# Optimization experiments

Measured on AMD Instinct MI355X. Metric: run time of the kernel, lower is better.

Reference implementation:

```python
import jax, jax.numpy as jnp
import numpy as np

D_IN, N_HEADS, N_KV, HEAD_DIM = 2048, 8, 4, 256
GROUP = N_HEADS // N_KV
SCALING = 256.0 ** -0.5  # query_pre_attn_scalar = 256
EPS = 1e-6


def _rms_norm(x, gamma):
    # Gemma-style RMSNorm with (1 + gamma) scale, over last dim (head_dim)
    var = jnp.mean(x * x, axis=-1, keepdims=True)
    return x * jax.lax.rsqrt(var + EPS) * (1.0 + gamma)


def _apply_rope(x, cos, sin):
    # x: [b, h, s, d]; cos/sin: [s, d] (rotate-half convention)
    d = x.shape[-1]
    x1, x2 = x[..., : d // 2], x[..., d // 2:]
    rotated = jnp.concatenate([-x2, x1], axis=-1)
    return x * cos[None, None] + rotated * sin[None, None]


def setup_inputs() -> dict:
    key = jax.random.key(0)
    ks = jax.random.split(key, 6)
    b, s = 2, 2048
    x = jax.random.normal(ks[0], (b, s, D_IN), dtype=jnp.float32)
    # causal mask: True above diagonal = masked
    mask = jnp.triu(jnp.ones((s, s), dtype=bool), k=1)
    # RoPE tables (base 10000)
    inv_freq = 1.0 / (10000.0 ** (jnp.arange(0, HEAD_DIM, 2, dtype=jnp.float32) / HEAD_DIM))
    angles = jnp.arange(s, dtype=jnp.float32)[:, None] * inv_freq[None, :]  # [s, d/2]
    angles = jnp.concatenate([angles, angles], axis=-1)  # [s, d]
    cos, sin = jnp.cos(angles), jnp.sin(angles)
    std = 0.02
    wq = jax.random.normal(ks[1], (N_HEADS * HEAD_DIM, D_IN), dtype=jnp.float32) * std
    wk = jax.random.normal(ks[2], (N_KV * HEAD_DIM, D_IN), dtype=jnp.float32) * std
    wv = jax.random.normal(ks[3], (N_KV * HEAD_DIM, D_IN), dtype=jnp.float32) * std
    wo = jax.random.normal(ks[4], (D_IN, N_HEADS * HEAD_DIM), dtype=jnp.float32) * std
    q_gamma = jnp.zeros((HEAD_DIM,), dtype=jnp.float32)
    k_gamma = jnp.zeros((HEAD_DIM,), dtype=jnp.float32)
    return {"x": x, "mask": mask, "cos": cos, "sin": sin,
            "wq": wq, "wk": wk, "wv": wv, "wo": wo,
            "q_gamma": q_gamma, "k_gamma": k_gamma}


def reference(x, mask, cos, sin, wq, wk, wv, wo, q_gamma, k_gamma):
    b, s, _ = x.shape
    # projections (torch Linear: y = x @ W.T)
    q = (x @ wq.T).reshape(b, s, N_HEADS, HEAD_DIM).transpose(0, 2, 1, 3)  # [b,H,s,d]
    k = (x @ wk.T).reshape(b, s, N_KV, HEAD_DIM).transpose(0, 2, 1, 3)     # [b,G,s,d]
    v = (x @ wv.T).reshape(b, s, N_KV, HEAD_DIM).transpose(0, 2, 1, 3)     # [b,G,s,d]
    q = _rms_norm(q, q_gamma)
    k = _rms_norm(k, k_gamma)
    q = _apply_rope(q, cos, sin) * SCALING
    k = _apply_rope(k, cos, sin)
    # GQA via broadcast (avoids repeat_interleave): head h = g*GROUP + j (group-major)
    qg = q.reshape(b, N_KV, GROUP, s, HEAD_DIM)
    scores = jnp.einsum('bgjqd,bgkd->bgjqk', qg, k)  # [b,G,group,s,s]
    scores = jnp.where(mask[None, None, None], -jnp.inf, scores)
    weights = jax.nn.softmax(scores, axis=-1)
    ctx = jnp.einsum('bgjqk,bgkd->bgjqd', weights, v)  # [b,G,group,s,d]
    ctx = ctx.reshape(b, N_HEADS, s, HEAD_DIM).transpose(0, 2, 1, 3).reshape(b, s, N_HEADS * HEAD_DIM)
    return ctx @ wo.T
```

## Files before the change

kernel.cpp:

```cpp
#include <hip/hip_runtime.h>
#include <math.h>


typedef __bf16 bf16x8 __attribute__((ext_vector_type(8)));
typedef __bf16 bf16x4 __attribute__((ext_vector_type(4)));
typedef float  f32x4  __attribute__((ext_vector_type(4)));

#define MFMA16(a, b, c) __builtin_amdgcn_mfma_f32_16x16x32_bf16(a, b, c, 0, 0, 0)

__device__ __forceinline__ void async16(const __bf16* g, const __bf16* l) {
  __builtin_amdgcn_global_load_lds(
      (__attribute__((address_space(1))) const void*)g,
      (__attribute__((address_space(3))) void*)l, 16, 0, 0);
}

__global__ __launch_bounds__(256) void cast_f32_bf16(
    const float* __restrict__ src, __bf16* __restrict__ dst) {
  const size_t i = ((size_t)blockIdx.x * 256 + threadIdx.x) * 4;
  f32x4 v = *(const f32x4*)(src + i);
  bf16x4 o;
#pragma unroll
  for (int j = 0; j < 4; j++) o[j] = (__bf16)v[j];
  *(bf16x4*)(dst + i) = o;
}

template <typename OT>
__device__ __forceinline__ void gemm_body(const __bf16* A, const __bf16* B,
                                          OT* C, size_t m0, size_t n0,
                                          size_t ccol0, int ldc) {
  constexpr int K = 2048;
  __shared__ __align__(16) __bf16 As[128 * 32];
  __shared__ __align__(16) __bf16 Bs[128 * 32];
  const int tid = threadIdx.x;
  const int wave = tid >> 6, lane = tid & 63;
  const int lr = lane & 15, lq = lane >> 4;
  const int wm = (wave >> 1) * 64, wn = (wave & 1) * 64;

  f32x4 acc[4][4];
#pragma unroll
  for (int i = 0; i < 4; i++)
#pragma unroll
    for (int j = 0; j < 4; j++)
#pragma unroll
      for (int r = 0; r < 4; r++) acc[i][j][r] = 0.f;

  int srow[2], skof[2];
#pragma unroll
  for (int c = 0; c < 2; c++) {
    const int t = wave * 2 + c;
    const int g = t * 8 + (lane >> 3);
    const int cc = (lane & 7) ^ (g & 7);
    srow[c] = g * 2 + (cc >> 2);
    skof[c] = (cc & 3) * 8;
  }

  for (int k0 = 0; k0 < K; k0 += 32) {
#pragma unroll
    for (int c = 0; c < 2; c++) {
      const int t = wave * 2 + c;
      async16(A + (m0 + srow[c]) * K + k0 + skof[c], As + t * 512);
      async16(B + (n0 + srow[c]) * K + k0 + skof[c], Bs + t * 512);
    }
    __syncthreads();
    bf16x8 af[4], bf[4];
#pragma unroll
    for (int i = 0; i < 4; i++) {
      const int row = wm + i * 16 + lr;
      const int g = row >> 1;
      const int p = ((row & 1) * 4 + lq) ^ (g & 7);
      af[i] = *(const bf16x8*)&As[g * 64 + p * 8];
    }
#pragma unroll
    for (int j = 0; j < 4; j++) {
      const int row = wn + j * 16 + lr;
      const int g = row >> 1;
      const int p = ((row & 1) * 4 + lq) ^ (g & 7);
      bf[j] = *(const bf16x8*)&Bs[g * 64 + p * 8];
    }
#pragma unroll
    for (int i = 0; i < 4; i++)
#pragma unroll
      for (int j = 0; j < 4; j++)
        acc[i][j] = MFMA16(af[i], bf[j], acc[i][j]);
    __syncthreads();
  }

#pragma unroll
  for (int i = 0; i < 4; i++)
#pragma unroll
    for (int j = 0; j < 4; j++)
#pragma unroll
      for (int r = 0; r < 4; r++) {
        const size_t row = m0 + wm + i * 16 + lq * 4 + r;
        const size_t col = ccol0 + wn + j * 16 + lr;
        C[row * (size_t)ldc + col] = (OT)acc[i][j][r];
      }
}

template <typename OT>
__global__ __launch_bounds__(256) void gemm_bt(
    const __bf16* __restrict__ A, const __bf16* __restrict__ B,
    OT* __restrict__ C, const int ldc) {
  gemm_body<OT>(A, B, C, (size_t)blockIdx.y * 128, (size_t)blockIdx.x * 128,
                (size_t)blockIdx.x * 128, ldc);
}

__global__ __launch_bounds__(512, 2) void gemm_qkv8(
    const __bf16* __restrict__ A, const __bf16* __restrict__ Bq,
    const __bf16* __restrict__ Bk, const __bf16* __restrict__ Bv,
    __bf16* __restrict__ C) {
  constexpr int NT = 32;
  __shared__ __align__(16) __bf16 As[2][256 * 64];
  __shared__ __align__(16) __bf16 Bs[2][256 * 64];

  const int bx = blockIdx.x;
  const __bf16* Bg;
  int nl;
  if (bx < 8)       { Bg = Bq; nl = bx; }
  else if (bx < 12) { Bg = Bk; nl = bx - 8; }
  else              { Bg = Bv; nl = bx - 12; }
  const size_t m0 = (size_t)blockIdx.y * 256;
  const size_t n0 = (size_t)nl * 256;
  const size_t ccol0 = (size_t)bx * 256;

  const int tid = threadIdx.x;
  const int wave = tid >> 6, lane = tid & 63;
  const int lr = lane & 15, lq = lane >> 4;
  const int wm = (wave >> 2) * 128, wn = (wave & 3) * 64;

  f32x4 acc[8][4];
#pragma unroll
  for (int i = 0; i < 8; i++)
#pragma unroll
    for (int j = 0; j < 4; j++)
#pragma unroll
      for (int r = 0; r < 4; r++) acc[i][j][r] = 0.f;

  const int srow0 = wave * 8 + (lane >> 3);
  const int sc = ((lane & 7) ^ (srow0 & 7)) * 8;

#define QSTAGE(kt_, nb_)                                                     \
  {                                                                          \
    const int k0_ = (kt_)*64;                                                \
    _Pragma("unroll") for (int s = 0; s < 4; s++) {                          \
      async16(A + (m0 + s * 64 + srow0) * 2048 + k0_ + sc,                   \
              &As[nb_][s * 4096 + wave * 512]);                              \
      async16(Bg + (n0 + s * 64 + srow0) * 2048 + k0_ + sc,                  \
              &Bs[nb_][s * 4096 + wave * 512]);                              \
    }                                                                        \
  }

  QSTAGE(0, 0);
  __syncthreads();

  for (int t = 0; t < NT; t++) {
    const int nb = t & 1;
    bf16x8 bf[8];
#pragma unroll
    for (int q = 0; q < 4; q++) {
      bf16x8 af[4];
#pragma unroll
      for (int di = 0; di < 2; di++)
#pragma unroll
        for (int kk = 0; kk < 2; kk++) {
          const int r = wm + q * 32 + di * 16 + lr;
          af[di * 2 + kk] =
              *(const bf16x8*)&As[nb][r * 64 + (((kk * 4 + lq) ^ (r & 7)) * 8)];
        }
      if (q == 0) {
#pragma unroll
        for (int nj = 0; nj < 4; nj++)
#pragma unroll
          for (int kk = 0; kk < 2; kk++) {
            const int r = wn + nj * 16 + lr;
            bf[nj * 2 + kk] = *(const bf16x8*)&Bs[nb][r * 64 +
                                (((kk * 4 + lq) ^ (r & 7)) * 8)];
          }
        if (t + 1 < NT) QSTAGE(t + 1, nb ^ 1);
      }
      __builtin_amdgcn_s_barrier();
      asm volatile("s_waitcnt lgkmcnt(0)" ::: "memory");
      __builtin_amdgcn_sched_barrier(0);
      __builtin_amdgcn_s_setprio(1);
#pragma unroll
      for (int di = 0; di < 2; di++)
#pragma unroll
        for (int nj = 0; nj < 4; nj++)
#pragma unroll
          for (int kk = 0; kk < 2; kk++)
            acc[q * 2 + di][nj] =
                MFMA16(af[di * 2 + kk], bf[nj * 2 + kk], acc[q * 2 + di][nj]);
      __builtin_amdgcn_s_setprio(0);
      if (q == 3)
        asm volatile("s_waitcnt vmcnt(0)" ::: "memory");
      __builtin_amdgcn_s_barrier();
    }
  }
#undef QSTAGE

#pragma unroll
  for (int i = 0; i < 8; i++)
#pragma unroll
    for (int j = 0; j < 4; j++)
#pragma unroll
      for (int r = 0; r < 4; r++) {
        const size_t row = m0 + wm + i * 16 + lq * 4 + r;
        const size_t col = ccol0 + wn + j * 16 + lr;
        C[row * 4096 + col] = (__bf16)acc[i][j][r];
      }
}

__global__ __launch_bounds__(256) void rmsrope(
    const __bf16* __restrict__ qkv, const float* __restrict__ cosb,
    const float* __restrict__ sinb, const float* __restrict__ qg,
    const float* __restrict__ kg, __bf16* __restrict__ qrot,
    __bf16* __restrict__ krot) {
  const int wave = threadIdx.x >> 6, lane = threadIdx.x & 63;
  const int rid = blockIdx.x * 4 + wave;
  const int m = rid / 12, seg = rid % 12;
  const int b = m >> 11, pos = m & 2047;
  const bool isq = seg < 8;
  const int col = isq ? seg * 256 : 2048 + (seg - 8) * 256;
  const int d = lane * 4;

  bf16x4 xv = *(const bf16x4*)(qkv + (size_t)m * 4096 + col + d);
  float x[4];
#pragma unroll
  for (int i = 0; i < 4; i++) x[i] = (float)xv[i];
  float ss = x[0] * x[0] + x[1] * x[1] + x[2] * x[2] + x[3] * x[3];
#pragma unroll
  for (int off = 1; off < 64; off <<= 1) ss += __shfl_xor(ss, off);
  const float inv = rsqrtf(ss * (1.f / 256.f) + 1e-6f);

  f32x4 gv = *(const f32x4*)((isq ? qg : kg) + d);
  float xn[4];
#pragma unroll
  for (int i = 0; i < 4; i++) xn[i] = x[i] * inv * (1.f + gv[i]);
  float rot[4];
#pragma unroll
  for (int i = 0; i < 4; i++) {
    const float pn = __shfl_xor(xn[i], 32);
    rot[i] = (lane < 32) ? -pn : pn;
  }
  f32x4 cv = *(const f32x4*)(cosb + (size_t)pos * 256 + d);
  f32x4 sv = *(const f32x4*)(sinb + (size_t)pos * 256 + d);
  const float sc = isq ? 0.0625f : 1.f;
  bf16x4 ov;
#pragma unroll
  for (int i = 0; i < 4; i++)
    ov[i] = (__bf16)((xn[i] * cv[i] + rot[i] * sv[i]) * sc);
  __bf16* dst = isq
      ? qrot + ((size_t)(b * 8 + seg) * 2048 + pos) * 256 + d
      : krot + ((size_t)(b * 4 + (seg - 8)) * 2048 + pos) * 256 + d;
  *(bf16x4*)dst = ov;
}

__global__ __launch_bounds__(256) void vtrans(const __bf16* __restrict__ qkv,
                                              __bf16* __restrict__ vT) {
  __shared__ __bf16 tile[64 * 65];
  const int bkv = blockIdx.z;
  const int d0 = blockIdx.y * 64, p0 = blockIdx.x * 64;
  const int t = threadIdx.x;
  const int b = bkv >> 2, kv = bkv & 3;
#pragma unroll
  for (int i = 0; i < 16; i++) {
    const int f = i * 256 + t;
    const int pl = f >> 6, dl = f & 63;
    tile[pl * 65 + dl] =
        qkv[(size_t)(b * 2048 + p0 + pl) * 4096 + 3072 + kv * 256 + d0 + dl];
  }
  __syncthreads();
#pragma unroll
  for (int i = 0; i < 16; i++) {
    const int f = i * 256 + t;
    const int dl = f >> 6, pl = f & 63;
    vT[((size_t)bkv * 256 + d0 + dl) * 2048 + p0 + pl] = tile[pl * 65 + dl];
  }
}

__global__ __launch_bounds__(128) void flash(
    const __bf16* __restrict__ qrot, const __bf16* __restrict__ krot,
    const __bf16* __restrict__ vT, __bf16* __restrict__ ctx) {
  __shared__ __align__(16) __bf16 Ks[64 * 256];
  __shared__ __align__(16) __bf16 Vs[256 * 64];
  __shared__ __align__(16) __bf16 Ps[2 * 32 * 64];
  const int tid = threadIdx.x, wave = tid >> 6, lane = tid & 63;
  const int lr = lane & 15, lq = lane >> 4;
  const int qt = (int)gridDim.x - 1 - (int)blockIdx.x;
  const int h = blockIdx.y, b = blockIdx.z, kv = h >> 1;
  const int q0 = qt * 64 + wave * 32;

  bf16x8 qf[2][8];
  {
    const __bf16* qbb = qrot + (size_t)(b * 8 + h) * 2048 * 256;
#pragma unroll
    for (int qi = 0; qi < 2; qi++)
#pragma unroll
      for (int i = 0; i < 8; i++)
        qf[qi][i] = *(const bf16x8*)(qbb + (size_t)(q0 + qi * 16 + lr) * 256 +
                                     i * 32 + lq * 8);
  }
  f32x4 acc[2][16];
#pragma unroll
  for (int qi = 0; qi < 2; qi++)
#pragma unroll
    for (int j = 0; j < 16; j++)
#pragma unroll
      for (int r = 0; r < 4; r++) acc[qi][j][r] = 0.f;
  float lsum[2][4];
#pragma unroll
  for (int qi = 0; qi < 2; qi++)
#pragma unroll
    for (int r = 0; r < 4; r++) lsum[qi][r] = 0.f;

  const __bf16* kbase = krot + (size_t)(b * 4 + kv) * 2048 * 256;
  const __bf16* vbase = vT + (size_t)(b * 4 + kv) * 256 * 2048;

  int koff[16], voff[16];
#pragma unroll
  for (int c = 0; c < 16; c++) {
    const int t = wave * 16 + c;
    {
      const int row = t * 2 + (lane >> 5);
      const int ch = (lane & 31) ^ (row & 31);
      koff[c] = row * 256 + ch * 8;
    }
    {
      const int d = t * 8 + (lane >> 3);
      const int ch = (lane & 7) ^ (d & 7);
      voff[c] = d * 2048 + ch * 8;
    }
  }

  for (int kt = 0; kt <= qt; kt++) {
    const int k0 = kt * 64;
#pragma unroll
    for (int c = 0; c < 16; c++) {
      const int t = wave * 16 + c;
      async16(kbase + (size_t)k0 * 256 + koff[c], Ks + t * 512);
      async16(vbase + k0 + voff[c], Vs + t * 512);
    }
    __syncthreads();

    f32x4 s[2][4];
#pragma unroll
    for (int qi = 0; qi < 2; qi++)
#pragma unroll
      for (int f = 0; f < 4; f++)
#pragma unroll
        for (int r = 0; r < 4; r++) s[qi][f][r] = 0.f;
#pragma unroll
    for (int i = 0; i < 8; i++) {
      bf16x8 kf[4];
#pragma unroll
      for (int f = 0; f < 4; f++) {
        const int row = f * 16 + lr;
        const int pch = (i * 4 + lq) ^ (row & 31);
        kf[f] = *(const bf16x8*)&Ks[row * 256 + pch * 8];
      }
#pragma unroll
      for (int qi = 0; qi < 2; qi++)
#pragma unroll
        for (int f = 0; f < 4; f++)
          s[qi][f] = MFMA16(qf[qi][i], kf[f], s[qi][f]);
    }

    const bool diag = (kt == qt);
#pragma unroll
    for (int qi = 0; qi < 2; qi++) {
      const int qa = q0 + qi * 16 + lq * 4;
#pragma unroll
      for (int f = 0; f < 4; f++) {
        const int ka = k0 + f * 16 + lr;
        const int row = qi * 16 + lq * 4;
        const int pchb = (f * 2 + (lr >> 3));
#pragma unroll
        for (int r = 0; r < 4; r++) {
          float p = __expf(s[qi][f][r] - 16.f);
          if (diag && ka > qa + r) p = 0.f;
          lsum[qi][r] += p;
          Ps[wave * 2048 + (row + r) * 64 + (pchb ^ ((row + r) & 7)) * 8 +
             (lr & 7)] = (__bf16)p;
        }
      }
    }
    asm volatile("s_waitcnt lgkmcnt(0)" ::: "memory");

#pragma unroll
    for (int m = 0; m < 2; m++) {
      bf16x8 pf[2];
#pragma unroll
      for (int qi = 0; qi < 2; qi++) {
        const int row = qi * 16 + lr;
        const int pch = (m * 4 + lq) ^ (row & 7);
        pf[qi] = *(const bf16x8*)&Ps[wave * 2048 + row * 64 + pch * 8];
      }
#pragma unroll
      for (int j = 0; j < 16; j++) {
        const int d = j * 16 + lr;
        const int pch = (m * 4 + lq) ^ (d & 7);
        bf16x8 vf = *(const bf16x8*)&Vs[d * 64 + pch * 8];
#pragma unroll
        for (int qi = 0; qi < 2; qi++)
          acc[qi][j] = MFMA16(pf[qi], vf, acc[qi][j]);
      }
    }
    __syncthreads();
  }

  float inv[2][4];
#pragma unroll
  for (int qi = 0; qi < 2; qi++)
#pragma unroll
    for (int r = 0; r < 4; r++) {
      float l = lsum[qi][r];
#pragma unroll
      for (int off = 1; off < 16; off <<= 1) l += __shfl_xor(l, off);
      inv[qi][r] = 1.f / l;
    }
#pragma unroll
  for (int qi = 0; qi < 2; qi++)
#pragma unroll
    for (int j = 0; j < 16; j++)
#pragma unroll
      for (int r = 0; r < 4; r++) {
        const int row = q0 + qi * 16 + lq * 4 + r;
        ctx[((size_t)(b * 2048 + row) * 8 + h) * 256 + j * 16 + lr] =
            (__bf16)(acc[qi][j][r] * inv[qi][r]);
      }
}

extern "C" void kernel_launch(void* const* d_in, const int* in_sizes, int n_in,
                              void* d_out, int out_size, void* d_ws,
                              size_t ws_size, hipStream_t stream) {
  const float* x = (const float*)d_in[0];
  const float* cosb = (const float*)d_in[2];
  const float* sinb = (const float*)d_in[3];
  const float* wq = (const float*)d_in[4];
  const float* wk = (const float*)d_in[5];
  const float* wv = (const float*)d_in[6];
  const float* wo = (const float*)d_in[7];
  const float* qg = (const float*)d_in[8];
  const float* kg = (const float*)d_in[9];
  float* out = (float*)d_out;

  char* ws = (char*)d_ws;
  __bf16* xbf = (__bf16*)ws;
  __bf16* wqbf = (__bf16*)(ws + ((size_t)16 << 20));
  __bf16* wkbf = (__bf16*)(ws + ((size_t)24 << 20));
  __bf16* wvbf = (__bf16*)(ws + ((size_t)28 << 20));
  __bf16* qkv = (__bf16*)(ws + ((size_t)32 << 20));
  __bf16* qrot = (__bf16*)ws;
  __bf16* krot = (__bf16*)(ws + ((size_t)16 << 20));
  __bf16* vTp = (__bf16*)(ws + ((size_t)24 << 20));
  __bf16* wobf = (__bf16*)(ws + ((size_t)32 << 20));
  __bf16* ctx = (__bf16*)(ws + ((size_t)40 << 20));

  cast_f32_bf16<<<8192, 256, 0, stream>>>(x, xbf);
  cast_f32_bf16<<<4096, 256, 0, stream>>>(wq, wqbf);
  cast_f32_bf16<<<2048, 256, 0, stream>>>(wk, wkbf);
  cast_f32_bf16<<<2048, 256, 0, stream>>>(wv, wvbf);

  gemm_qkv8<<<dim3(16, 16), 512, 0, stream>>>(xbf, wqbf, wkbf, wvbf, qkv);

  rmsrope<<<12288, 256, 0, stream>>>(qkv, cosb, sinb, qg, kg, qrot, krot);
  vtrans<<<dim3(32, 4, 8), 256, 0, stream>>>(qkv, vTp);

  cast_f32_bf16<<<4096, 256, 0, stream>>>(wo, wobf);
  flash<<<dim3(32, 8, 2), 128, 0, stream>>>(qrot, krot, vTp, ctx);

  gemm_bt<float><<<dim3(16, 32), 256, 0, stream>>>(ctx, wobf, out, 2048);
}
```

Baseline: 405.0 us.

## Pipeline output projection GEMM, fuse input casts, vectorize V transpose

The output projection GEMM moves from a simple 128x128, K=32 single-buffered kernel to a 512-thread, 128x256 tile, K=64 double-buffered kernel with async LDS loads, swizzled layout and setprio scheduling, modeled on the QKV GEMM. The four separate fp32-to-bf16 cast launches become one fused launch, and the V transpose kernel now uses 16-byte vector loads and stores. The goal is better MFMA utilization in the final GEMM and less launch and memory-access overhead. The larger tiles yield a grid of only 256 blocks, which may underfill the device.

Result: faster. 396.0 us (-2.2%).

```diff
diff --git a/kernel.cpp b/kernel.cpp
--- a/kernel.cpp
+++ b/kernel.cpp
@@ -12,6 +12,27 @@
   __builtin_amdgcn_global_load_lds(
       (__attribute__((address_space(1))) const void*)g,
       (__attribute__((address_space(3))) void*)l, 16, 0, 0);
+}
+
+__global__ __launch_bounds__(256) void cast_fused(
+    const float* __restrict__ x, const float* __restrict__ wq,
+    const float* __restrict__ wk, const float* __restrict__ wv,
+    __bf16* __restrict__ xbf, __bf16* __restrict__ wqbf,
+    __bf16* __restrict__ wkbf, __bf16* __restrict__ wvbf) {
+  const int bx = blockIdx.x;
+  const float* src;
+  __bf16* dst;
+  int b0;
+  if (bx < 8192)       { src = x;  dst = xbf;  b0 = 0; }
+  else if (bx < 12288) { src = wq; dst = wqbf; b0 = 8192; }
+  else if (bx < 14336) { src = wk; dst = wkbf; b0 = 12288; }
+  else                 { src = wv; dst = wvbf; b0 = 14336; }
+  const size_t i = ((size_t)(bx - b0) * 256 + threadIdx.x) * 4;
+  f32x4 v = *(const f32x4*)(src + i);
+  bf16x4 o;
+#pragma unroll
+  for (int j = 0; j < 4; j++) o[j] = (__bf16)v[j];
+  *(bf16x4*)(dst + i) = o;
 }
 
 __global__ __launch_bounds__(256) void cast_f32_bf16(
@@ -22,87 +43,6 @@
 #pragma unroll
   for (int j = 0; j < 4; j++) o[j] = (__bf16)v[j];
   *(bf16x4*)(dst + i) = o;
-}
-
-template <typename OT>
-__device__ __forceinline__ void gemm_body(const __bf16* A, const __bf16* B,
-                                          OT* C, size_t m0, size_t n0,
-                                          size_t ccol0, int ldc) {
-  constexpr int K = 2048;
-  __shared__ __align__(16) __bf16 As[128 * 32];
-  __shared__ __align__(16) __bf16 Bs[128 * 32];
-  const int tid = threadIdx.x;
-  const int wave = tid >> 6, lane = tid & 63;
-  const int lr = lane & 15, lq = lane >> 4;
-  const int wm = (wave >> 1) * 64, wn = (wave & 1) * 64;
-
-  f32x4 acc[4][4];
-#pragma unroll
-  for (int i = 0; i < 4; i++)
-#pragma unroll
-    for (int j = 0; j < 4; j++)
-#pragma unroll
-      for (int r = 0; r < 4; r++) acc[i][j][r] = 0.f;
-
-  int srow[2], skof[2];
-#pragma unroll
-  for (int c = 0; c < 2; c++) {
-    const int t = wave * 2 + c;
-    const int g = t * 8 + (lane >> 3);
-    const int cc = (lane & 7) ^ (g & 7);
-    srow[c] = g * 2 + (cc >> 2);
-    skof[c] = (cc & 3) * 8;
-  }
-
-  for (int k0 = 0; k0 < K; k0 += 32) {
-#pragma unroll
-    for (int c = 0; c < 2; c++) {
-      const int t = wave * 2 + c;
-      async16(A + (m0 + srow[c]) * K + k0 + skof[c], As + t * 512);
-      async16(B + (n0 + srow[c]) * K + k0 + skof[c], Bs + t * 512);
-    }
-    __syncthreads();
-    bf16x8 af[4], bf[4];
-#pragma unroll
-    for (int i = 0; i < 4; i++) {
-      const int row = wm + i * 16 + lr;
-      const int g = row >> 1;
-      const int p = ((row & 1) * 4 + lq) ^ (g & 7);
-      af[i] = *(const bf16x8*)&As[g * 64 + p * 8];
-    }
-#pragma unroll
-    for (int j = 0; j < 4; j++) {
-      const int row = wn + j * 16 + lr;
-      const int g = row >> 1;
-      const int p = ((row & 1) * 4 + lq) ^ (g & 7);
-      bf[j] = *(const bf16x8*)&Bs[g * 64 + p * 8];
-    }
-#pragma unroll
-    for (int i = 0; i < 4; i++)
-#pragma unroll
-      for (int j = 0; j < 4; j++)
-        acc[i][j] = MFMA16(af[i], bf[j], acc[i][j]);
-    __syncthreads();
-  }
-
-#pragma unroll
-  for (int i = 0; i < 4; i++)
-#pragma unroll
-    for (int j = 0; j < 4; j++)
-#pragma unroll
-      for (int r = 0; r < 4; r++) {
-        const size_t row = m0 + wm + i * 16 + lq * 4 + r;
-        const size_t col = ccol0 + wn + j * 16 + lr;
-        C[row * (size_t)ldc + col] = (OT)acc[i][j][r];
-      }
-}
-
-template <typename OT>
-__global__ __launch_bounds__(256) void gemm_bt(
-    const __bf16* __restrict__ A, const __bf16* __restrict__ B,
-    OT* __restrict__ C, const int ldc) {
-  gemm_body<OT>(A, B, C, (size_t)blockIdx.y * 128, (size_t)blockIdx.x * 128,
-                (size_t)blockIdx.x * 128, ldc);
 }
 
 __global__ __launch_bounds__(512, 2) void gemm_qkv8(
@@ -207,6 +147,103 @@
         const size_t row = m0 + wm + i * 16 + lq * 4 + r;
         const size_t col = ccol0 + wn + j * 16 + lr;
         C[row * 4096 + col] = (__bf16)acc[i][j][r];
+      }
+}
+
+__global__ __launch_bounds__(512, 2) void gemm_bt8(
+    const __bf16* __restrict__ A, const __bf16* __restrict__ B,
+    float* __restrict__ C) {
+  constexpr int NT = 32;
+  __shared__ __align__(16) __bf16 As[2][128 * 64];
+  __shared__ __align__(16) __bf16 Bs[2][256 * 64];
+
+  const size_t m0 = (size_t)blockIdx.y * 128;
+  const size_t n0 = (size_t)blockIdx.x * 256;
+
+  const int tid = threadIdx.x;
+  const int wave = tid >> 6, lane = tid & 63;
+  const int lr = lane & 15, lq = lane >> 4;
+  const int wm = (wave >> 2) * 64, wn = (wave & 3) * 64;
+
+  f32x4 acc[4][4];
+#pragma unroll
+  for (int i = 0; i < 4; i++)
+#pragma unroll
+    for (int j = 0; j < 4; j++)
+#pragma unroll
+      for (int r = 0; r < 4; r++) acc[i][j][r] = 0.f;
+
+  const int srow0 = wave * 8 + (lane >> 3);
+  const int sc = ((lane & 7) ^ (srow0 & 7)) * 8;
+
+#define BSTAGE(kt_, nb_)                                                     \
+  {                                                                          \
+    const int k0_ = (kt_)*64;                                                \
+    _Pragma("unroll") for (int s = 0; s < 2; s++)                            \
+      async16(A + (m0 + s * 64 + srow0) * 2048 + k0_ + sc,                   \
+              &As[nb_][s * 4096 + wave * 512]);                              \
+    _Pragma("unroll") for (int s = 0; s < 4; s++)                            \
+      async16(B + (n0 + s * 64 + srow0) * 2048 + k0_ + sc,                   \
+              &Bs[nb_][s * 4096 + wave * 512]);                              \
+  }
+
+  BSTAGE(0, 0);
+  __syncthreads();
+
+  for (int t = 0; t < NT; t++) {
+    const int nb = t & 1;
+    bf16x8 bf[8];
+#pragma unroll
+    for (int p = 0; p < 2; p++) {
+      bf16x8 af[4];
+#pragma unroll
+      for (int di = 0; di < 2; di++)
+#pragma unroll
+        for (int kk = 0; kk < 2; kk++) {
+          const int r = wm + p * 32 + di * 16 + lr;
+          af[di * 2 + kk] =
+              *(const bf16x8*)&As[nb][r * 64 + (((kk * 4 + lq) ^ (r & 7)) * 8)];
+        }
+      if (p == 0) {
+#pragma unroll
+        for (int nj = 0; nj < 4; nj++)
+#pragma unroll
+          for (int kk = 0; kk < 2; kk++) {
+            const int r = wn + nj * 16 + lr;
+            bf[nj * 2 + kk] = *(const bf16x8*)&Bs[nb][r * 64 +
+                                (((kk * 4 + lq) ^ (r & 7)) * 8)];
+          }
+        if (t + 1 < NT) BSTAGE(t + 1, nb ^ 1);
+      }
+      __builtin_amdgcn_s_barrier();
+      asm volatile("s_waitcnt lgkmcnt(0)" ::: "memory");
+      __builtin_amdgcn_sched_barrier(0);
+      __builtin_amdgcn_s_setprio(1);
+#pragma unroll
+      for (int di = 0; di < 2; di++)
+#pragma unroll
+        for (int nj = 0; nj < 4; nj++)
+#pragma unroll
+          for (int kk = 0; kk < 2; kk++)
+            acc[p * 2 + di][nj] =
+                MFMA16(af[di * 2 + kk], bf[nj * 2 + kk], acc[p * 2 + di][nj]);
+      __builtin_amdgcn_s_setprio(0);
+      if (p == 1)
+        asm volatile("s_waitcnt vmcnt(0)" ::: "memory");
+      __builtin_amdgcn_s_barrier();
+    }
+  }
+#undef BSTAGE
+
+#pragma unroll
+  for (int i = 0; i < 4; i++)
+#pragma unroll
+    for (int j = 0; j < 4; j++)
+#pragma unroll
+      for (int r = 0; r < 4; r++) {
+        const size_t row = m0 + wm + i * 16 + lq * 4 + r;
+        const size_t col = n0 + wn + j * 16 + lr;
+        C[row * 2048 + col] = acc[i][j][r];
       }
 }
 
@@ -263,18 +300,23 @@
   const int t = threadIdx.x;
   const int b = bkv >> 2, kv = bkv & 3;
 #pragma unroll
-  for (int i = 0; i < 16; i++) {
+  for (int i = 0; i < 2; i++) {
     const int f = i * 256 + t;
-    const int pl = f >> 6, dl = f & 63;
-    tile[pl * 65 + dl] =
-        qkv[(size_t)(b * 2048 + p0 + pl) * 4096 + 3072 + kv * 256 + d0 + dl];
+    const int pl = f >> 3, dc = (f & 7) * 8;
+    bf16x8 v = *(const bf16x8*)(qkv + (size_t)(b * 2048 + p0 + pl) * 4096 +
+                                3072 + kv * 256 + d0 + dc);
+#pragma unroll
+    for (int e = 0; e < 8; e++) tile[pl * 65 + dc + e] = v[e];
   }
   __syncthreads();
 #pragma unroll
-  for (int i = 0; i < 16; i++) {
+  for (int i = 0; i < 2; i++) {
     const int f = i * 256 + t;
-    const int dl = f >> 6, pl = f & 63;
-    vT[((size_t)bkv * 256 + d0 + dl) * 2048 + p0 + pl] = tile[pl * 65 + dl];
+    const int dl = f >> 3, pc = (f & 7) * 8;
+    bf16x8 o;
+#pragma unroll
+    for (int e = 0; e < 8; e++) o[e] = tile[(pc + e) * 65 + dl];
+    *(bf16x8*)(vT + ((size_t)bkv * 256 + d0 + dl) * 2048 + p0 + pc) = o;
   }
 }
 
@@ -456,10 +498,7 @@
   __bf16* wobf = (__bf16*)(ws + ((size_t)32 << 20));
   __bf16* ctx = (__bf16*)(ws + ((size_t)40 << 20));
 
-  cast_f32_bf16<<<8192, 256, 0, stream>>>(x, xbf);
-  cast_f32_bf16<<<4096, 256, 0, stream>>>(wq, wqbf);
-  cast_f32_bf16<<<2048, 256, 0, stream>>>(wk, wkbf);
-  cast_f32_bf16<<<2048, 256, 0, stream>>>(wv, wvbf);
+  cast_fused<<<16384, 256, 0, stream>>>(x, wq, wk, wv, xbf, wqbf, wkbf, wvbf);
 
   gemm_qkv8<<<dim3(16, 16), 512, 0, stream>>>(xbf, wqbf, wkbf, wvbf, qkv);
 
@@ -469,5 +508,5 @@
   cast_f32_bf16<<<4096, 256, 0, stream>>>(wo, wobf);
   flash<<<dim3(32, 8, 2), 128, 0, stream>>>(qrot, krot, vTp, ctx);
 
-  gemm_bt<float><<<dim3(16, 32), 256, 0, stream>>>(ctx, wobf, out, 2048);
-}
+  gemm_bt8<<<dim3(8, 32), 512, 0, stream>>>(ctx, wobf, out);
+}
```
